# Optimization experiments

Measured on AMD Instinct MI355X. Metric: run time of the kernel, lower is better.

The kernel has to match this reference:

```python
import jax, jax.numpy as jnp
import numpy as np

C = 512
HEADS = 8
HEAD_DIM = C // HEADS
GROUPS = 32
EPS = 1e-5


def group_norm(x, scale, bias):
    b, c, h, w = x.shape
    xg = x.reshape(b, GROUPS, -1)
    mean = xg.mean(axis=-1, keepdims=True)
    var = xg.var(axis=-1, keepdims=True)
    xg = (xg - mean) * jax.lax.rsqrt(var + EPS)
    x = xg.reshape(b, c, h, w)
    return x * scale[None, :, None, None] + bias[None, :, None, None]


def conv1x1(x, w, b):
    # w: (out_c, in_c), x: (B, C, H, W)
    return jnp.einsum('oc,bchw->bohw', w, x) + b[None, :, None, None]


def setup_inputs() -> dict:
    key = jax.random.key(0)
    ks = jax.random.split(key, 11)
    s = 1.0 / np.sqrt(C)
    return {
        'x': jax.random.normal(ks[0], (8, C, 32, 32), jnp.float32),
        'gn_scale': jnp.ones((C,), jnp.float32),
        'gn_bias': jnp.zeros((C,), jnp.float32),
        'wq': jax.random.normal(ks[1], (C, C), jnp.float32) * s,
        'bq': jax.random.normal(ks[2], (C,), jnp.float32) * 0.01,
        'wk': jax.random.normal(ks[3], (C, C), jnp.float32) * s,
        'bk': jax.random.normal(ks[4], (C,), jnp.float32) * 0.01,
        'wv': jax.random.normal(ks[5], (C, C), jnp.float32) * s,
        'bv': jax.random.normal(ks[6], (C,), jnp.float32) * 0.01,
        'wp': jax.random.normal(ks[7], (C, C), jnp.float32) * s,
        'bp': jax.random.normal(ks[8], (C,), jnp.float32) * 0.01,
    }


def reference(x, gn_scale, gn_bias, wq, bq, wk, bk, wv, bv, wp, bp):
    b, c, h, w = x.shape
    n = h * w
    h_in = x
    xn = group_norm(x, gn_scale, gn_bias)
    q = conv1x1(xn, wq, bq).reshape(b, HEADS, HEAD_DIM, n)
    k = conv1x1(xn, wk, bk).reshape(b, HEADS, HEAD_DIM, n)
    v = conv1x1(xn, wv, bv).reshape(b, HEADS, HEAD_DIM, n)
    scale = 1.0 / np.sqrt(HEAD_DIM).astype(np.float32)
    attn = jnp.einsum('bhcn,bhcm->bhnm', q, k) * scale
    attn = jax.nn.softmax(attn, axis=-1)
    out = jnp.einsum('bhnm,bhcm->bhcn', attn, v)
    out = out.reshape(b, c, h, w)
    out = conv1x1(out, wp, bp)
    return out + h_in
```

## Files before the change

kernel.cpp:

```cpp
#include <hip/hip_runtime.h>

#define CC 512
#define NN 1024
#define NB 8
#define NH 8
#define HD 64

typedef __attribute__((ext_vector_type(8))) short s16x8;
typedef __attribute__((ext_vector_type(4))) short s16x4;
typedef __attribute__((ext_vector_type(4))) float f32x4;
typedef __attribute__((ext_vector_type(16))) float f32x16;

__device__ __forceinline__ unsigned cvtpk(float lo, float hi){
  unsigned r;
  asm("v_cvt_pk_bf16_f32 %0, %1, %2" : "=v"(r) : "v"(lo), "v"(hi));
  return r;
}

__device__ __forceinline__ s16x4 pack4(float a, float b, float c, float d){
  union { unsigned u[2]; s16x4 v; } r;
  r.u[0] = cvtpk(a, b);
  r.u[1] = cvtpk(c, d);
  return r.v;
}

__device__ __forceinline__ void gload16(const void* g, void* l){
  __builtin_amdgcn_global_load_lds((const __attribute__((address_space(1))) void*)g,
                                   (__attribute__((address_space(3))) void*)l, 16, 0, 0);
}

__global__ __launch_bounds__(256) void prep_kernel(const float* __restrict__ x,
    const float* __restrict__ gsc, const float* __restrict__ gbi,
    const float* __restrict__ w0, const float* __restrict__ w1,
    const float* __restrict__ w2, const float* __restrict__ w3,
    short* __restrict__ wbf, short* __restrict__ xnt){
  if (blockIdx.x < 1024){
    const int i = blockIdx.x*256 + threadIdx.x;
    const int sel = i >> 16;
    const int off = (i & 65535) << 2;
    const float* src = (sel==0) ? w0 : (sel==1) ? w1 : (sel==2) ? w2 : w3;
    const float4 v = *reinterpret_cast<const float4*>(src + off);
    *reinterpret_cast<s16x4*>(wbf + (size_t)sel*262144 + off) = pack4(v.x, v.y, v.z, v.w);
    return;
  }
  const int blk = blockIdx.x - 1024;
  const int b = blk >> 5;
  const int g = blk & 31;
  const int t = threadIdx.x;
  const float* base = x + ((size_t)b*CC + g*16)*NN;
  float4 vals[16];
  float s = 0.f, s2 = 0.f;
  #pragma unroll
  for (int k = 0; k < 16; ++k){
    float4 v = *reinterpret_cast<const float4*>(base + k*NN + t*4);
    vals[k] = v;
    s  += v.x + v.y + v.z + v.w;
    s2 += v.x*v.x + v.y*v.y + v.z*v.z + v.w*v.w;
  }
  #pragma unroll
  for (int m = 1; m < 64; m <<= 1){ s += __shfl_xor(s, m); s2 += __shfl_xor(s2, m); }
  __shared__ float rs[4], rs2[4];
  const int wid = t >> 6, lane = t & 63;
  if (lane == 0){ rs[wid] = s; rs2[wid] = s2; }
  __syncthreads();
  s  = rs[0] + rs[1] + rs[2] + rs[3];
  s2 = rs2[0] + rs2[1] + rs2[2] + rs2[3];
  const float mean = s * (1.f/16384.f);
  const float inv = rsqrtf(s2 * (1.f/16384.f) - mean*mean + 1e-5f);
  float scl[16], off[16];
  #pragma unroll
  for (int k = 0; k < 16; ++k){
    const float sc = gsc[g*16 + k] * inv;
    scl[k] = sc;
    off[k] = gbi[g*16 + k] - mean * sc;
  }
  short* obase = xnt + ((size_t)b*NN + t*4)*CC + g*16;
  #pragma unroll
  for (int i = 0; i < 4; ++i){
    float fv[16];
    #pragma unroll
    for (int k = 0; k < 16; ++k){
      const float v = (i==0) ? vals[k].x : (i==1) ? vals[k].y : (i==2) ? vals[k].z : vals[k].w;
      fv[k] = v * scl[k] + off[k];
    }
    union { unsigned u[4]; s16x8 v; } lo, hi;
    #pragma unroll
    for (int j = 0; j < 4; ++j){
      lo.u[j] = cvtpk(fv[2*j],     fv[2*j + 1]);
      hi.u[j] = cvtpk(fv[8 + 2*j], fv[8 + 2*j + 1]);
    }
    *reinterpret_cast<s16x8*>(obase + (size_t)i*CC)     = lo.v;
    *reinterpret_cast<s16x8*>(obase + (size_t)i*CC + 8) = hi.v;
  }
}

__global__ __launch_bounds__(256) void gemm_qkv(
    const short* __restrict__ Wb, const short* __restrict__ Bmat,
    const float* __restrict__ bias0, const float* __restrict__ bias1, const float* __restrict__ bias2,
    short* __restrict__ qt, short* __restrict__ kt2, short* __restrict__ vo)
{
  const int w = blockIdx.x;
  const int nt = w & 7;
  const int s = w >> 3;
  const int batch = s & 7;
  const int r = s >> 3;
  const int mt = r & 3, z = r >> 2;
  const int tid = threadIdx.x;
  const int lane = tid & 63, wid = tid >> 6;
  const int wm = wid >> 1, wn = wid & 1;

  __shared__ short As[2][128*32];
  __shared__ short Bs[2][128*32];

  const short* Wz = Wb + (size_t)z * 262144;
  const short* Brow = Bmat + ((size_t)batch*NN + nt*128)*CC;

  const f32x4 fzero = {0.f, 0.f, 0.f, 0.f};
  f32x4 acc[4][4];
  #pragma unroll
  for (int i = 0; i < 4; ++i)
  #pragma unroll
  for (int j = 0; j < 4; ++j)
    acc[i][j] = fzero;

  const int srow = tid >> 2, sh = tid & 3;
  const int sg = sh ^ ((srow >> 1) & 3);
  const short* gaBase = Wz + (size_t)(mt*128 + srow)*CC + sg*8;
  const short* gbBase = Brow + (size_t)srow*CC + sg*8;

  auto stage = [&](int kk, int buf){
    const short* ga = gaBase + kk*32;
    const short* gb = gbBase + kk*32;
    gload16(ga,         &As[buf][tid*8]);
    gload16(ga + 64*CC, &As[buf][(tid + 256)*8]);
    gload16(gb,         &Bs[buf][tid*8]);
    gload16(gb + 64*CC, &Bs[buf][(tid + 256)*8]);
  };

  const int rch = (lane >> 4) ^ (((lane & 15) >> 1) & 3);

  auto compute = [&](int buf){
    s16x8 a[4], b[4];
    #pragma unroll
    for (int mi = 0; mi < 4; ++mi){
      const int row = wm*64 + mi*16 + (lane & 15);
      a[mi] = *reinterpret_cast<const s16x8*>(&As[buf][row*32 + rch*8]);
    }
    #pragma unroll
    for (int ni = 0; ni < 4; ++ni){
      const int row = wn*64 + ni*16 + (lane & 15);
      b[ni] = *reinterpret_cast<const s16x8*>(&Bs[buf][row*32 + rch*8]);
    }
    if (z == 2){
      #pragma unroll
      for (int mi = 0; mi < 4; ++mi)
      #pragma unroll
      for (int ni = 0; ni < 4; ++ni)
        acc[mi][ni] = __builtin_amdgcn_mfma_f32_16x16x32_bf16(b[ni], a[mi], acc[mi][ni], 0, 0, 0);
    } else {
      #pragma unroll
      for (int mi = 0; mi < 4; ++mi)
      #pragma unroll
      for (int ni = 0; ni < 4; ++ni)
        acc[mi][ni] = __builtin_amdgcn_mfma_f32_16x16x32_bf16(a[mi], b[ni], acc[mi][ni], 0, 0, 0);
    }
  };

  stage(0, 0);
  asm volatile("s_waitcnt vmcnt(0)" ::: "memory");
  __builtin_amdgcn_s_barrier();
  int buf = 0;
  #pragma unroll
  for (int kk = 0; kk < 16; ++kk){
    if (kk < 15) stage(kk + 1, buf ^ 1);
    compute(buf);
    if (kk < 15){
      asm volatile("s_waitcnt vmcnt(0)" ::: "memory");
      __builtin_amdgcn_s_barrier();
    }
    buf ^= 1;
  }

  const int obase = mt*128 + wm*64;
  const int head = mt*2 + wm;
  const size_t hb = ((size_t)batch*NH + head)*65536;
  const int hi2 = (lane >> 5) & 1;
  const int j0 = ((lane >> 4) & 1)*4;
  if (z < 2){
    const float* bias = (z == 0) ? bias0 : bias1;
    short* dst = (z == 0) ? qt : kt2;
    const float qs = (z == 0) ? 0.125f * 1.44269504f : 1.0f;
    #pragma unroll
    for (int mi = 0; mi < 4; ++mi){
      float bv4[4];
      #pragma unroll
      for (int r2 = 0; r2 < 4; ++r2) bv4[r2] = bias[obase + mi*16 + (lane>>4)*4 + r2];
      #pragma unroll
      for (int ni = 0; ni < 4; ++ni){
        const int l = (ni & 1)*16 + (lane & 15) + 32*hi2;
        const int q5 = nt*4 + wn*2 + (ni >> 1);
        const s16x4 pk = pack4((acc[mi][ni][0] + bv4[0]) * qs,
                               (acc[mi][ni][1] + bv4[1]) * qs,
                               (acc[mi][ni][2] + bv4[2]) * qs,
                               (acc[mi][ni][3] + bv4[3]) * qs);
        *reinterpret_cast<s16x4*>(dst + hb + (size_t)((q5*4 + mi)*64 + l)*8 + j0) = pk;
      }
    }
  } else {
    #pragma unroll
    for (int mi = 0; mi < 4; ++mi){
      const float bv = bias2[obase + mi*16 + (lane & 15)];
      const int ci = mi >> 1;
      const int cl = (mi & 1)*16 + (lane & 15);
      #pragma unroll
      for (int ni = 0; ni < 4; ++ni){
        const int m5 = nt*2 + wn;
        const s16x4 pk = pack4(acc[mi][ni][0] + bv, acc[mi][ni][1] + bv,
                               acc[mi][ni][2] + bv, acc[mi][ni][3] + bv);
        *reinterpret_cast<s16x4*>(vo + hb + (size_t)((((ci*16 + m5)*4 + ni)*64) + cl + 32*hi2)*8 + j0) = pk;
      }
    }
  }
}

__global__ __launch_bounds__(256) void gemm_proj(
    const short* __restrict__ Wb, const short* __restrict__ Bmat,
    const float* __restrict__ bias0, const float* __restrict__ resid,
    float* __restrict__ outp)
{
  const int w = blockIdx.x;
  const int nt = w & 7;
  const int s = w >> 3;
  const int batch = s & 7;
  const int mt = s >> 3;
  const int tid = threadIdx.x;
  const int lane = tid & 63, wid = tid >> 6;
  const int wm = wid >> 1, wn = wid & 1;

  __shared__ short As[2][128*32];
  __shared__ short Bs[2][128*32];

  const short* Wz = Wb + (size_t)3 * 262144;
  const short* Brow = Bmat + ((size_t)batch*NN + nt*128)*CC;

  const f32x4 fzero = {0.f, 0.f, 0.f, 0.f};
  f32x4 acc[4][4];
  #pragma unroll
  for (int i = 0; i < 4; ++i)
  #pragma unroll
  for (int j = 0; j < 4; ++j)
    acc[i][j] = fzero;

  const int srow = tid >> 2, sh = tid & 3;
  const int sg = sh ^ ((srow >> 1) & 3);
  const short* gaBase = Wz + (size_t)(mt*128 + srow)*CC + sg*8;
  const short* gbBase = Brow + (size_t)srow*CC + sg*8;

  auto stage = [&](int kk, int buf){
    const short* ga = gaBase + kk*32;
    const short* gb = gbBase + kk*32;
    gload16(ga,         &As[buf][tid*8]);
    gload16(ga + 64*CC, &As[buf][(tid + 256)*8]);
    gload16(gb,         &Bs[buf][tid*8]);
    gload16(gb + 64*CC, &Bs[buf][(tid + 256)*8]);
  };

  const int rch = (lane >> 4) ^ (((lane & 15) >> 1) & 3);

  auto compute = [&](int buf){
    s16x8 a[4], b[4];
    #pragma unroll
    for (int mi = 0; mi < 4; ++mi){
      const int row = wm*64 + mi*16 + (lane & 15);
      a[mi] = *reinterpret_cast<const s16x8*>(&As[buf][row*32 + rch*8]);
    }
    #pragma unroll
    for (int ni = 0; ni < 4; ++ni){
      const int row = wn*64 + ni*16 + (lane & 15);
      b[ni] = *reinterpret_cast<const s16x8*>(&Bs[buf][row*32 + rch*8]);
    }
    #pragma unroll
    for (int mi = 0; mi < 4; ++mi)
    #pragma unroll
    for (int ni = 0; ni < 4; ++ni)
      acc[mi][ni] = __builtin_amdgcn_mfma_f32_16x16x32_bf16(b[ni], a[mi], acc[mi][ni], 0, 0, 0);
  };

  stage(0, 0);
  asm volatile("s_waitcnt vmcnt(0)" ::: "memory");
  __builtin_amdgcn_s_barrier();
  int buf = 0;
  #pragma unroll
  for (int kk = 0; kk < 16; ++kk){
    if (kk < 15) stage(kk + 1, buf ^ 1);
    compute(buf);
    if (kk < 15){
      asm volatile("s_waitcnt vmcnt(0)" ::: "memory");
      __builtin_amdgcn_s_barrier();
    }
    buf ^= 1;
  }

  const int obase = mt*128 + wm*64;
  const int nbase = nt*128 + wn*64;
  #pragma unroll
  for (int mi = 0; mi < 4; ++mi){
    const int o = obase + mi*16 + (lane & 15);
    const float bv = bias0[o];
    #pragma unroll
    for (int ni = 0; ni < 4; ++ni){
      const int n4 = nbase + ni*16 + (lane >> 4)*4;
      const size_t idx = ((size_t)batch*CC + o)*NN + n4;
      const float4 rv = *reinterpret_cast<const float4*>(resid + idx);
      float4 ov;
      ov.x = acc[mi][ni][0] + bv + rv.x;
      ov.y = acc[mi][ni][1] + bv + rv.y;
      ov.z = acc[mi][ni][2] + bv + rv.z;
      ov.w = acc[mi][ni][3] + bv + rv.w;
      *reinterpret_cast<float4*>(outp + idx) = ov;
    }
  }
}

__global__ __launch_bounds__(256, 2) void attn_kernel(
    const short* __restrict__ qp, const short* __restrict__ kp, const short* __restrict__ vp,
    short* __restrict__ ot)
{
  const int bid = blockIdx.x;
  const int xcd = bid & 7, rr = bid >> 3;
  const int bh  = xcd*8 + (rr & 7);
  const int qt  = rr >> 3;
  const int b = bh >> 3, head = bh & 7;
  const int tid = threadIdx.x, lane = tid & 63, wid = tid >> 6;
  const int col = lane & 31;
  const int qg = wid & 1, kh = wid >> 1;
  const int q0 = qt*64 + qg*32;

  const short* Qf = qp + (size_t)bh*65536;
  const short* Kf = kp + (size_t)bh*65536;
  const short* Vf = vp + (size_t)bh*65536;

  __shared__ float Lof[2][32][64];
  __shared__ float Ll[2][64];

  const int q5 = qt*2 + qg;
  s16x8 qf[4];
  #pragma unroll
  for (int ks = 0; ks < 4; ++ks)
    qf[ks] = *reinterpret_cast<const s16x8*>(Qf + (size_t)(q5*4 + ks)*512 + lane*8);

  f32x16 of0, of1;
  #pragma unroll
  for (int r = 0; r < 16; ++r){ of0[r] = 0.f; of1[r] = 0.f; }
  float l = 0.f;

  auto kload = [&](int itn, s16x8 (&kf)[2][4]){
    const short* kb = Kf + (size_t)(kh*16 + itn*2)*2048 + lane*8;
    #pragma unroll
    for (int t = 0; t < 2; ++t)
      #pragma unroll
      for (int ks = 0; ks < 4; ++ks)
        kf[t][ks] = *reinterpret_cast<const s16x8*>(kb + t*2048 + ks*512);
  };

  auto vload = [&](int itn, s16x8 (&vf)[2][4]){
    const short* vb = Vf + (size_t)(kh*8 + itn)*2048 + lane*8;
    #pragma unroll
    for (int ci = 0; ci < 2; ++ci)
      #pragma unroll
      for (int s = 0; s < 4; ++s)
        vf[ci][s] = *reinterpret_cast<const s16x8*>(vb + ci*32768 + s*512);
  };

  auto pack = [&](f32x16& sv, s16x8& p0, s16x8& p1){
    union { unsigned u[4]; s16x8 v; } w0, w1;
    {
      unsigned a = cvtpk(sv[0], sv[1]);
      unsigned c = cvtpk(sv[4], sv[5]);
      auto r = __builtin_amdgcn_permlane32_swap(a, c, false, false);
      w0.u[0] = r[0]; w0.u[2] = r[1];
      a = cvtpk(sv[2], sv[3]);
      c = cvtpk(sv[6], sv[7]);
      r = __builtin_amdgcn_permlane32_swap(a, c, false, false);
      w0.u[1] = r[0]; w0.u[3] = r[1];
    }
    {
      unsigned a = cvtpk(sv[8], sv[9]);
      unsigned c = cvtpk(sv[12], sv[13]);
      auto r = __builtin_amdgcn_permlane32_swap(a, c, false, false);
      w1.u[0] = r[0]; w1.u[2] = r[1];
      a = cvtpk(sv[10], sv[11]);
      c = cvtpk(sv[14], sv[15]);
      r = __builtin_amdgcn_permlane32_swap(a, c, false, false);
      w1.u[1] = r[0]; w1.u[3] = r[1];
    }
    p0 = w0.v; p1 = w1.v;
  };

  auto body = [&](int it, s16x8 (&kf)[2][4], s16x8 (&kfn)[2][4],
                          s16x8 (&vf)[2][4], s16x8 (&vfn)[2][4]){
    f32x16 s0, s1;
    #pragma unroll
    for (int r = 0; r < 16; ++r){ s0[r] = 0.f; s1[r] = 0.f; }
    #pragma unroll
    for (int ks = 0; ks < 4; ++ks){
      s0 = __builtin_amdgcn_mfma_f32_32x32x16_bf16(kf[0][ks], qf[ks], s0, 0, 0, 0);
      s1 = __builtin_amdgcn_mfma_f32_32x32x16_bf16(kf[1][ks], qf[ks], s1, 0, 0, 0);
    }
    if (it < 7) kload(it + 1, kfn);
    #pragma unroll
    for (int r = 0; r < 16; ++r){ s0[r] = __builtin_amdgcn_exp2f(s0[r]); }
    #pragma unroll
    for (int r = 0; r < 16; ++r){ s1[r] = __builtin_amdgcn_exp2f(s1[r]); }
    float t[16];
    #pragma unroll
    for (int r = 0; r < 16; ++r) t[r] = s0[r] + s1[r];
    #pragma unroll
    for (int o = 8; o > 0; o >>= 1)
      #pragma unroll
      for (int r = 0; r < 8; ++r) if (r < o) t[r] = t[r] + t[r + o];
    l += t[0] + __shfl_xor(t[0], 32);
    s16x8 pf[4];
    pack(s0, pf[0], pf[1]);
    pack(s1, pf[2], pf[3]);
    if (it < 7) vload(it + 1, vfn);
    #pragma unroll
    for (int s = 0; s < 4; ++s){
      of0 = __builtin_amdgcn_mfma_f32_32x32x16_bf16(vf[0][s], pf[s], of0, 0, 0, 0);
      of1 = __builtin_amdgcn_mfma_f32_32x32x16_bf16(vf[1][s], pf[s], of1, 0, 0, 0);
    }
  };

  s16x8 kfA[2][4], kfB[2][4];
  s16x8 vfA[2][4], vfB[2][4];
  kload(0, kfA);
  vload(0, vfA);
  #pragma unroll 1
  for (int ii = 0; ii < 4; ++ii){
    body(2*ii,     kfA, kfB, vfA, vfB);
    body(2*ii + 1, kfB, kfA, vfB, vfA);
  }

  __syncthreads();
  if (kh == 1){
    #pragma unroll
    for (int r = 0; r < 16; ++r){
      Lof[qg][r][lane]      = of0[r];
      Lof[qg][16 + r][lane] = of1[r];
    }
    Ll[qg][lane] = l;
  }
  __syncthreads();
  if (kh == 0){
    const float linv = 1.f / (l + Ll[qg][lane]);
    const int hi = lane >> 5;
    const int n = q0 + col;
    short* ob = ot + ((size_t)b*NN + n)*CC + head*HD + hi*4;
    #pragma unroll
    for (int rq = 0; rq < 4; ++rq){
      s16x4 pk = pack4((of0[rq*4 + 0] + Lof[qg][rq*4 + 0][lane]) * linv,
                       (of0[rq*4 + 1] + Lof[qg][rq*4 + 1][lane]) * linv,
                       (of0[rq*4 + 2] + Lof[qg][rq*4 + 2][lane]) * linv,
                       (of0[rq*4 + 3] + Lof[qg][rq*4 + 3][lane]) * linv);
      *reinterpret_cast<s16x4*>(ob + rq*8) = pk;
      pk = pack4((of1[rq*4 + 0] + Lof[qg][16 + rq*4 + 0][lane]) * linv,
                 (of1[rq*4 + 1] + Lof[qg][16 + rq*4 + 1][lane]) * linv,
                 (of1[rq*4 + 2] + Lof[qg][16 + rq*4 + 2][lane]) * linv,
                 (of1[rq*4 + 3] + Lof[qg][16 + rq*4 + 3][lane]) * linv);
      *reinterpret_cast<s16x4*>(ob + 32 + rq*8) = pk;
    }
  }
}

extern "C" void kernel_launch(void* const* d_in, const int* in_sizes, int n_in,
                              void* d_out, int out_size, void* d_ws, size_t ws_size,
                              hipStream_t stream) {
  const float* x   = (const float*)d_in[0];
  const float* gsc = (const float*)d_in[1];
  const float* gbi = (const float*)d_in[2];
  const float* wq  = (const float*)d_in[3];
  const float* bq  = (const float*)d_in[4];
  const float* wk  = (const float*)d_in[5];
  const float* bk  = (const float*)d_in[6];
  const float* wv  = (const float*)d_in[7];
  const float* bv  = (const float*)d_in[8];
  const float* wp  = (const float*)d_in[9];
  const float* bp  = (const float*)d_in[10];
  float* out = (float*)d_out;

  char* ws = (char*)d_ws;
  short* wbf = (short*)(ws);
  short* xnt = (short*)(ws + (2u<<20));
  short* qt  = (short*)(ws + (10u<<20));
  short* kt  = (short*)(ws + (18u<<20));
  short* v   = (short*)(ws + (26u<<20));
  short* aot = (short*)(ws + (34u<<20));

  prep_kernel<<<1280, 256, 0, stream>>>(x, gsc, gbi, wq, wk, wv, wp, wbf, xnt);
  gemm_qkv<<<dim3(768), 256, 0, stream>>>(wbf, xnt, bq, bk, bv, qt, kt, v);
  attn_kernel<<<dim3(1024), 256, 0, stream>>>(qt, kt, v, aot);
  gemm_proj<<<dim3(256), 256, 0, stream>>>(wbf, aot, bp, x, out);
}
```

Measured before the change: 77.80 us.

## Stage K/V tiles through shared memory and drop split-K reduction in attention

The attention kernel now has each block handle 128 queries (4 waves × 32) and loop over all 16 key tiles. K and V tiles are double-buffered in LDS via direct global-to-LDS loads, so all four waves share them instead of each wave loading K/V into registers. The old scheme split keys across two wave pairs and merged partial outputs through shared memory; that reduction is removed, and the grid is halved. The cost is a block barrier every iteration, fewer blocks for occupancy, and LDS read traffic.

```diff
diff --git a/kernel.cpp b/kernel.cpp
--- a/kernel.cpp
+++ b/kernel.cpp
@@ -327,23 +327,21 @@
     short* __restrict__ ot)
 {
   const int bid = blockIdx.x;
-  const int xcd = bid & 7, rr = bid >> 3;
-  const int bh  = xcd*8 + (rr & 7);
-  const int qt  = rr >> 3;
+  const int xcd = bid & 7, slot = bid >> 3;
+  const int bh  = xcd*8 + (slot & 7);
+  const int qt  = slot >> 3;
   const int b = bh >> 3, head = bh & 7;
   const int tid = threadIdx.x, lane = tid & 63, wid = tid >> 6;
   const int col = lane & 31;
-  const int qg = wid & 1, kh = wid >> 1;
-  const int q0 = qt*64 + qg*32;
 
   const short* Qf = qp + (size_t)bh*65536;
   const short* Kf = kp + (size_t)bh*65536;
   const short* Vf = vp + (size_t)bh*65536;
 
-  __shared__ float Lof[2][32][64];
-  __shared__ float Ll[2][64];
-
-  const int q5 = qt*2 + qg;
+  __shared__ short Ks[2][4096];
+  __shared__ short Vs[2][4096];
+
+  const int q5 = qt*4 + wid;
   s16x8 qf[4];
   #pragma unroll
   for (int ks = 0; ks < 4; ++ks)
@@ -354,22 +352,11 @@
   for (int r = 0; r < 16; ++r){ of0[r] = 0.f; of1[r] = 0.f; }
   float l = 0.f;
 
-  auto kload = [&](int itn, s16x8 (&kf)[2][4]){
-    const short* kb = Kf + (size_t)(kh*16 + itn*2)*2048 + lane*8;
-    #pragma unroll
-    for (int t = 0; t < 2; ++t)
-      #pragma unroll
-      for (int ks = 0; ks < 4; ++ks)
-        kf[t][ks] = *reinterpret_cast<const s16x8*>(kb + t*2048 + ks*512);
-  };
-
-  auto vload = [&](int itn, s16x8 (&vf)[2][4]){
-    const short* vb = Vf + (size_t)(kh*8 + itn)*2048 + lane*8;
-    #pragma unroll
-    for (int ci = 0; ci < 2; ++ci)
-      #pragma unroll
-      for (int s = 0; s < 4; ++s)
-        vf[ci][s] = *reinterpret_cast<const s16x8*>(vb + ci*32768 + s*512);
+  auto stage = [&](int it, int buf){
+    gload16(Kf + (size_t)it*4096 + tid*8,        &Ks[buf][tid*8]);
+    gload16(Kf + (size_t)it*4096 + 2048 + tid*8, &Ks[buf][2048 + tid*8]);
+    gload16(Vf + (size_t)it*2048 + tid*8,        &Vs[buf][tid*8]);
+    gload16(Vf + (size_t)(16 + it)*2048 + tid*8, &Vs[buf][2048 + tid*8]);
   };
 
   auto pack = [&](f32x16& sv, s16x8& p0, s16x8& p1){
@@ -397,8 +384,14 @@
     p0 = w0.v; p1 = w1.v;
   };
 
-  auto body = [&](int it, s16x8 (&kf)[2][4], s16x8 (&kfn)[2][4],
-                          s16x8 (&vf)[2][4], s16x8 (&vfn)[2][4]){
+  auto body = [&](int it, int buf){
+    s16x8 kf[2][4];
+    #pragma unroll
+    for (int t = 0; t < 2; ++t)
+      #pragma unroll
+      for (int ks = 0; ks < 4; ++ks)
+        kf[t][ks] = *reinterpret_cast<const s16x8*>(&Ks[buf][t*2048 + ks*512 + lane*8]);
+    if (it < 15) stage(it + 1, buf ^ 1);
     f32x16 s0, s1;
     #pragma unroll
     for (int r = 0; r < 16; ++r){ s0[r] = 0.f; s1[r] = 0.f; }
@@ -407,7 +400,6 @@
       s0 = __builtin_amdgcn_mfma_f32_32x32x16_bf16(kf[0][ks], qf[ks], s0, 0, 0, 0);
       s1 = __builtin_amdgcn_mfma_f32_32x32x16_bf16(kf[1][ks], qf[ks], s1, 0, 0, 0);
     }
-    if (it < 7) kload(it + 1, kfn);
     #pragma unroll
     for (int r = 0; r < 16; ++r){ s0[r] = __builtin_amdgcn_exp2f(s0[r]); }
     #pragma unroll
@@ -423,52 +415,45 @@
     s16x8 pf[4];
     pack(s0, pf[0], pf[1]);
     pack(s1, pf[2], pf[3]);
-    if (it < 7) vload(it + 1, vfn);
+    s16x8 vf[2][4];
+    #pragma unroll
+    for (int ci = 0; ci < 2; ++ci)
+      #pragma unroll
+      for (int s = 0; s < 4; ++s)
+        vf[ci][s] = *reinterpret_cast<const s16x8*>(&Vs[buf][ci*2048 + s*512 + lane*8]);
     #pragma unroll
     for (int s = 0; s < 4; ++s){
       of0 = __builtin_amdgcn_mfma_f32_32x32x16_bf16(vf[0][s], pf[s], of0, 0, 0, 0);
       of1 = __builtin_amdgcn_mfma_f32_32x32x16_bf16(vf[1][s], pf[s], of1, 0, 0, 0);
     }
-  };
-
-  s16x8 kfA[2][4], kfB[2][4];
-  s16x8 vfA[2][4], vfB[2][4];
-  kload(0, kfA);
-  vload(0, vfA);
+    if (it < 15){
+      __builtin_amdgcn_sched_barrier(0);
+      asm volatile("s_waitcnt vmcnt(0)" ::: "memory");
+      __builtin_amdgcn_s_barrier();
+    }
+  };
+
+  stage(0, 0);
+  asm volatile("s_waitcnt vmcnt(0)" ::: "memory");
+  __builtin_amdgcn_s_barrier();
   #pragma unroll 1
-  for (int ii = 0; ii < 4; ++ii){
-    body(2*ii,     kfA, kfB, vfA, vfB);
-    body(2*ii + 1, kfB, kfA, vfB, vfA);
-  }
-
-  __syncthreads();
-  if (kh == 1){
-    #pragma unroll
-    for (int r = 0; r < 16; ++r){
-      Lof[qg][r][lane]      = of0[r];
-      Lof[qg][16 + r][lane] = of1[r];
-    }
-    Ll[qg][lane] = l;
-  }
-  __syncthreads();
-  if (kh == 0){
-    const float linv = 1.f / (l + Ll[qg][lane]);
-    const int hi = lane >> 5;
-    const int n = q0 + col;
-    short* ob = ot + ((size_t)b*NN + n)*CC + head*HD + hi*4;
-    #pragma unroll
-    for (int rq = 0; rq < 4; ++rq){
-      s16x4 pk = pack4((of0[rq*4 + 0] + Lof[qg][rq*4 + 0][lane]) * linv,
-                       (of0[rq*4 + 1] + Lof[qg][rq*4 + 1][lane]) * linv,
-                       (of0[rq*4 + 2] + Lof[qg][rq*4 + 2][lane]) * linv,
-                       (of0[rq*4 + 3] + Lof[qg][rq*4 + 3][lane]) * linv);
-      *reinterpret_cast<s16x4*>(ob + rq*8) = pk;
-      pk = pack4((of1[rq*4 + 0] + Lof[qg][16 + rq*4 + 0][lane]) * linv,
-                 (of1[rq*4 + 1] + Lof[qg][16 + rq*4 + 1][lane]) * linv,
-                 (of1[rq*4 + 2] + Lof[qg][16 + rq*4 + 2][lane]) * linv,
-                 (of1[rq*4 + 3] + Lof[qg][16 + rq*4 + 3][lane]) * linv);
-      *reinterpret_cast<s16x4*>(ob + 32 + rq*8) = pk;
-    }
+  for (int ii = 0; ii < 8; ++ii){
+    body(2*ii,     0);
+    body(2*ii + 1, 1);
+  }
+
+  const float linv = 1.f / l;
+  const int hi = lane >> 5;
+  const int n = qt*128 + wid*32 + col;
+  short* ob = ot + ((size_t)b*NN + n)*CC + head*HD + hi*4;
+  #pragma unroll
+  for (int rq = 0; rq < 4; ++rq){
+    s16x4 pk = pack4(of0[rq*4 + 0] * linv, of0[rq*4 + 1] * linv,
+                     of0[rq*4 + 2] * linv, of0[rq*4 + 3] * linv);
+    *reinterpret_cast<s16x4*>(ob + rq*8) = pk;
+    pk = pack4(of1[rq*4 + 0] * linv, of1[rq*4 + 1] * linv,
+               of1[rq*4 + 2] * linv, of1[rq*4 + 3] * linv);
+    *reinterpret_cast<s16x4*>(ob + 32 + rq*8) = pk;
   }
 }
 
@@ -498,6 +483,6 @@
 
   prep_kernel<<<1280, 256, 0, stream>>>(x, gsc, gbi, wq, wk, wv, wp, wbf, xnt);
   gemm_qkv<<<dim3(768), 256, 0, stream>>>(wbf, xnt, bq, bk, bv, qt, kt, v);
-  attn_kernel<<<dim3(1024), 256, 0, stream>>>(qt, kt, v, aot);
+  attn_kernel<<<dim3(512), 256, 0, stream>>>(qt, kt, v, aot);
   gemm_proj<<<dim3(256), 256, 0, stream>>>(wbf, aot, bp, x, out);
 }
```

Result: faster. 74.52 us, median of 2 (-4.2%).
